# Performance work log

Hardware: AMD Instinct MI355X
Metric: run time of the kernel (lower is better)

## Reference

```python
import jax, jax.numpy as jnp
import numpy as np

DIM = 96
HEADS = 6
WS = 8                      # window_size
OWS = int(WS * 0.5) + WS    # overlap_win_size = 12
PAD = (OWS - WS) // 2       # 2
Dd = Hh = Ww = 24
B = 1
L = Dd * Hh * Ww
MLP_H = DIM * 2
TBL = (WS + OWS - 1) ** 3   # 6859 relative-position-bias entries


def setup_inputs() -> dict:
    key = jax.random.key(0)
    ks = jax.random.split(key, 8)
    def n(k, shape, s=0.02):
        return jax.random.normal(k, shape, jnp.float32) * s
    return {
        "x": jax.random.normal(ks[0], (B, L, DIM), jnp.float32),
        "ln1_w": jnp.ones((DIM,), jnp.float32),
        "ln1_b": jnp.zeros((DIM,), jnp.float32),
        "qkv_w": n(ks[1], (3 * DIM, DIM)),
        "qkv_b": jnp.zeros((3 * DIM,), jnp.float32),
        "rpb": n(ks[2], (TBL, HEADS)),
        "proj_w": n(ks[3], (DIM, DIM)),
        "proj_b": jnp.zeros((DIM,), jnp.float32),
        "ln2_w": jnp.ones((DIM,), jnp.float32),
        "ln2_b": jnp.zeros((DIM,), jnp.float32),
        "fc1_w": n(ks[4], (MLP_H, DIM)),
        "fc1_b": jnp.zeros((MLP_H,), jnp.float32),
        "fc2_w": n(ks[5], (DIM, MLP_H)),
        "fc2_b": jnp.zeros((DIM,), jnp.float32),
        "rpi": jax.random.randint(ks[6], (WS ** 3, OWS ** 3), 0, TBL),
        "D": Dd, "H": Hh, "W": Ww,
    }


def _ln(x, w, b):
    m = jnp.mean(x, -1, keepdims=True)
    v = jnp.var(x, -1, keepdims=True)
    return (x - m) / jnp.sqrt(v + 1e-5) * w + b


def _ocab3d(x, ln1_w, ln1_b, qkv_w, qkv_b, rpb, proj_w, proj_b,
            ln2_w, ln2_b, fc1_w, fc1_b, fc2_w, fc2_b, rpi, D, H, W):
    Bz, Lz, C = x.shape
    hd = C // HEADS
    scale = hd ** -0.5
    shortcut = x

    xn = _ln(x, ln1_w, ln1_b).reshape(Bz, D, H, W, C)
    qkv = xn @ qkv_w.T + qkv_b                   # [B,D,H,W,3C]
    q = qkv[..., :C]
    kv = qkv[..., C:]                            # cat(k, v) on channels, [B,D,H,W,2C]

    nD, nH, nW = D // WS, H // WS, W // WS
    nw = nD * nH * nW

    # non-overlapping query windows -> [B*nw, WS^3, C]
    qw = q.reshape(Bz, nD, WS, nH, WS, nW, WS, C)
    qw = qw.transpose(0, 1, 3, 5, 2, 4, 6, 7).reshape(Bz * nw, WS ** 3, C)

    # overlapping kv windows via pad + strided gather (mirrors F.pad + unfold)
    kvp = jnp.pad(kv, ((0, 0), (PAD, PAD), (PAD, PAD), (PAD, PAD), (0, 0)))
    idx_d = (jnp.arange(nD) * WS)[:, None] + jnp.arange(OWS)[None, :]
    idx_h = (jnp.arange(nH) * WS)[:, None] + jnp.arange(OWS)[None, :]
    idx_w = (jnp.arange(nW) * WS)[:, None] + jnp.arange(OWS)[None, :]
    kw = kvp[:, idx_d]                 # [B,nD,OWS,Hp,Wp,2C]
    kw = kw[:, :, :, idx_h]            # [B,nD,OWS,nH,OWS,Wp,2C]
    kw = kw[:, :, :, :, :, idx_w]      # [B,nD,OWS,nH,OWS,nW,OWS,2C]
    kw = kw.transpose(0, 1, 3, 5, 2, 4, 6, 7).reshape(Bz * nw, OWS ** 3, 2 * C)
    kk, vv = kw[..., :C], kw[..., C:]

    qh = qw.reshape(-1, WS ** 3, HEADS, hd).transpose(0, 2, 1, 3) * scale
    kh = kk.reshape(-1, OWS ** 3, HEADS, hd).transpose(0, 2, 1, 3)
    vh = vv.reshape(-1, OWS ** 3, HEADS, hd).transpose(0, 2, 1, 3)

    attn = jnp.einsum('bhqd,bhkd->bhqk', qh, kh)               # [B*nw,H,512,1728]
    bias = rpb[rpi.reshape(-1)].reshape(WS ** 3, OWS ** 3, HEADS).transpose(2, 0, 1)
    attn = jax.nn.softmax(attn + bias[None], axis=-1)
    out = jnp.einsum('bhqk,bhkd->bhqd', attn, vh)
    out = out.transpose(0, 2, 1, 3).reshape(Bz * nw, WS ** 3, C)

    # window reverse -> [B, L, C]
    out = out.reshape(Bz, nD, nH, nW, WS, WS, WS, C)
    out = out.transpose(0, 1, 4, 2, 5, 3, 6, 7).reshape(Bz, D * H * W, C)

    x2 = out @ proj_w.T + proj_b + shortcut
    h1 = jax.nn.gelu(_ln(x2, ln2_w, ln2_b) @ fc1_w.T + fc1_b, approximate=False)
    return x2 + (h1 @ fc2_w.T + fc2_b)


def reference(x, ln1_w, ln1_b, qkv_w, qkv_b, rpb, proj_w, proj_b,
              ln2_w, ln2_b, fc1_w, fc1_b, fc2_w, fc2_b, rpi, D, H, W):
    return _ocab3d(x, ln1_w, ln1_b, qkv_w, qkv_b, rpb, proj_w, proj_b,
                   ln2_w, ln2_b, fc1_w, fc1_b, fc2_w, fc2_b, rpi, D, H, W)
```

## Files before the change

kernel.cpp:

```cpp
#include <hip/hip_runtime.h>
#include <math.h>

#define DIMC   96
#define NHEADS 6
#define HD     16
#define WSZ    8
#define OWSZ   12
#define PADW   2
#define DD     24
#define LTOK   13824
#define NWIN   27
#define NKEY   1728
#define NROW   512
#define MLPH   192
#define PDIM   28
#define PD3    21952
#define TBL    6859
#define LSTR   82944
#define AOSTR  1327104
#define LOG2E  1.4426950408889634f

typedef __attribute__((ext_vector_type(4))) short bf16x4;
typedef __attribute__((ext_vector_type(8))) short bf16x8;
typedef __attribute__((ext_vector_type(4))) float f32x4;

__device__ __forceinline__ unsigned short bfround(float f) {
    unsigned u = __float_as_uint(f);
    return (unsigned short)((u + 0x7FFFu + ((u >> 16) & 1u)) >> 16);
}
__device__ __forceinline__ unsigned bfpack(float a, float b) {
    unsigned ua = __float_as_uint(a), ub = __float_as_uint(b);
    ua = (ua + 0x7FFFu + ((ua >> 16) & 1u)) >> 16;
    ub = (ub + 0x7FFFu + ((ub >> 16) & 1u)) >> 16;
    return ua | (ub << 16);
}
__device__ __forceinline__ uint4 pack8(const float* v) {
    uint4 u;
    u.x = bfpack(v[0], v[1]); u.y = bfpack(v[2], v[3]);
    u.z = bfpack(v[4], v[5]); u.w = bfpack(v[6], v[7]);
    return u;
}
__device__ __forceinline__ bf16x4 pack4(f32x4 p) {
    union { uint2 u; bf16x4 v; } r;
    r.u.x = __builtin_amdgcn_perm(__float_as_uint(p[1]), __float_as_uint(p[0]), 0x07060302u);
    r.u.y = __builtin_amdgcn_perm(__float_as_uint(p[3]), __float_as_uint(p[2]), 0x07060302u);
    return r.v;
}
__device__ __forceinline__ f32x4 cvt4(uint2 b) {
    f32x4 c;
    c[0] = __uint_as_float(b.x << 16);
    c[1] = __uint_as_float(b.x & 0xffff0000u);
    c[2] = __uint_as_float(b.y << 16);
    c[3] = __uint_as_float(b.y & 0xffff0000u);
    return c;
}
__device__ __forceinline__ f32x4 mfma16(bf16x4 a, bf16x4 b, f32x4 c) {
#if __has_builtin(__builtin_amdgcn_mfma_f32_16x16x16bf16_1k)
    return __builtin_amdgcn_mfma_f32_16x16x16bf16_1k(a, b, c, 0, 0, 0);
#else
    bf16x8 a8 = {a[0], a[1], a[2], a[3], 0, 0, 0, 0};
    bf16x8 b8 = {b[0], b[1], b[2], b[3], 0, 0, 0, 0};
    return __builtin_amdgcn_mfma_f32_16x16x32_bf16(a8, b8, c, 0, 0, 0);
#endif
}
__device__ __forceinline__ f32x4 mfma32k(bf16x8 a, bf16x8 b, f32x4 c) {
    return __builtin_amdgcn_mfma_f32_16x16x32_bf16(a, b, c, 0, 0, 0);
}
__device__ __forceinline__ float fexp2(float x) {
#if __has_builtin(__builtin_amdgcn_exp2f)
    return __builtin_amdgcn_exp2f(x);
#else
    return exp2f(x);
#endif
}

#define QKVB 1296
#define ZB   515
#define WPB  45
#define BIASB 216
__global__ __launch_bounds__(256) void qkvz_kernel(
        const float* __restrict__ X, const float* __restrict__ W,
        const float* __restrict__ bias, const float* __restrict__ lnw,
        const float* __restrict__ lnb,
        const float* __restrict__ projw, const float* __restrict__ fc1w,
        const float* __restrict__ fc2w,
        const int* __restrict__ rpi, const float* __restrict__ rpb,
        unsigned short* __restrict__ q16, unsigned short* __restrict__ kvp2,
        uint4* __restrict__ wpack, unsigned short* __restrict__ biasP) {
    __shared__ uint4 Af4[2 * 3 * 4 * 16];
    __shared__ uint4 Bf4[6 * 3 * 4 * 16];
    int bx = blockIdx.x, tid = threadIdx.x;

    if (bx >= QKVB + ZB + WPB) {
        int b2 = bx - (QKVB + ZB + WPB);
        int c  = b2 % 27;
        int qp = b2 / 27;
        int quart = qp >> 1, qt = qp & 1;
        int wavep = tid >> 6, quadp = (tid >> 4) & 3, m16p = tid & 15;
        int q = quart * 128 + wavep * 32 + qt * 16 + m16p;
        const int* rp = rpi + (long)q * NKEY + c * 64 + quadp * 8;
        #pragma unroll
        for (int kt = 0; kt < 4; ++kt) {
            int4 t = *(const int4*)(rp + (kt >> 1) * 32 + (kt & 1) * 4);
            const float2* p0 = (const float2*)(rpb + (long)t.x * 6);
            const float2* p1 = (const float2*)(rpb + (long)t.y * 6);
            const float2* p2 = (const float2*)(rpb + (long)t.z * 6);
            const float2* p3 = (const float2*)(rpb + (long)t.w * 6);
            #pragma unroll
            for (int hp = 0; hp < 3; ++hp) {
                float2 a0 = p0[hp], a1 = p1[hp], a2 = p2[hp], a3 = p3[hp];
                uint2 ua, ub;
                ua.x = bfpack(a0.x * LOG2E, a1.x * LOG2E);
                ua.y = bfpack(a2.x * LOG2E, a3.x * LOG2E);
                ub.x = bfpack(a0.y * LOG2E, a1.y * LOG2E);
                ub.y = bfpack(a2.y * LOG2E, a3.y * LOG2E);
                *(uint2*)(biasP + ((long)((2*hp)   * 4 + quart) * 27 + c) * 8192
                          + qt * 4096 + tid * 16 + kt * 4) = ua;
                *(uint2*)(biasP + ((long)((2*hp+1) * 4 + quart) * 27 + c) * 8192
                          + qt * 4096 + tid * 16 + kt * 4) = ub;
            }
        }
        return;
    }
    if (bx >= QKVB + ZB) {
        int u = (bx - QKVB - ZB) * 256 + tid;
        if (u < 5760) {
            int p = (u < 1152) ? u : (u < 3456 ? (u - 1152) % 1152 : (u - 3456) % 1152);
            int nn = p & 15, r = p >> 4, qg = r & 3, r2 = r >> 2;
            int kt = r2 % 3, ct = r2 / 3;
            int n = ct * 16 + nn, g = kt * 4 + qg;
            const float* src;
            if (u < 1152)      src = projw + n * 96 + g * 8;
            else if (u < 3456) { int nc = (u - 1152) / 1152; src = fc1w + (long)(nc * 96 + n) * 96 + g * 8; }
            else               { int kh = (u - 3456) / 1152; src = fc2w + (long)n * 192 + kh * 96 + g * 8; }
            const float4* s4 = (const float4*)src;
            float v[8];
            float4 t0 = s4[0], t1 = s4[1];
            v[0]=t0.x; v[1]=t0.y; v[2]=t0.z; v[3]=t0.w;
            v[4]=t1.x; v[5]=t1.y; v[6]=t1.z; v[7]=t1.w;
            wpack[u] = pack8(v);
        }
        return;
    }
    if (bx >= QKVB) {
        int t = (bx - QKVB) * 256 + tid;
        if (t < 21952 * 6) {
            int head = t / PD3, pos = t % PD3;
            int d = pos / 784, h = (pos / 28) % 28, w = pos % 28;
            if (d < 2 || d >= 26 || h < 2 || h >= 26 || w < 2 || w >= 26) {
                uint4* p = (uint4*)(kvp2 + ((long)head * PD3 + pos) * 32);
                uint4 z = make_uint4(0, 0, 0, 0);
                p[0] = z; p[1] = z; p[2] = z; p[3] = z;
            }
        }
        return;
    }

    int nc   = bx % 3;
    int row0 = (bx / 3) * 32;

    if (tid < 128) {
        int row = tid >> 2, part = tid & 3;
        int rt = row >> 4, mm = row & 15;
        float v[24];
        const float4* xp = (const float4*)(X + (long)(row0 + row) * 96 + part * 24);
        float s = 0.f, sq = 0.f;
        #pragma unroll
        for (int i = 0; i < 6; ++i) {
            float4 t = xp[i];
            v[i*4+0] = t.x; v[i*4+1] = t.y; v[i*4+2] = t.z; v[i*4+3] = t.w;
            s  += t.x + t.y + t.z + t.w;
            sq += t.x*t.x + t.y*t.y + t.z*t.z + t.w*t.w;
        }
        s  += __shfl_xor(s, 1);  s  += __shfl_xor(s, 2);
        sq += __shfl_xor(sq, 1); sq += __shfl_xor(sq, 2);
        float mean = s * (1.f / 96.f);
        float inv  = rsqrtf(sq * (1.f / 96.f) - mean * mean + 1e-5f);
        const float4* wp = (const float4*)(lnw + part * 24);
        const float4* bp = (const float4*)(lnb + part * 24);
        #pragma unroll
        for (int i = 0; i < 6; ++i) {
            float4 wv = wp[i], bv = bp[i];
            v[i*4+0] = (v[i*4+0] - mean) * inv * wv.x + bv.x;
            v[i*4+1] = (v[i*4+1] - mean) * inv * wv.y + bv.y;
            v[i*4+2] = (v[i*4+2] - mean) * inv * wv.z + bv.z;
            v[i*4+3] = (v[i*4+3] - mean) * inv * wv.w + bv.w;
        }
        #pragma unroll
        for (int gg = 0; gg < 3; ++gg) {
            int g = part * 3 + gg;
            int kt = g >> 2, qq = g & 3;
            Af4[((rt * 3 + kt) * 4 + qq) * 16 + mm] = pack8(v + gg * 8);
        }
    }
    for (int idx = tid; idx < 96 * 12; idx += 256) {
        int n = idx / 12;
        int g = idx % 12;
        const float4* wp = (const float4*)(W + (long)(nc * 96 + n) * 96 + g * 8);
        float v[8];
        float4 t0 = wp[0], t1 = wp[1];
        v[0]=t0.x; v[1]=t0.y; v[2]=t0.z; v[3]=t0.w;
        v[4]=t1.x; v[5]=t1.y; v[6]=t1.z; v[7]=t1.w;
        int ct = n >> 4, nn = n & 15, kt = g >> 2, qg = g & 3;
        Bf4[((ct * 3 + kt) * 4 + qg) * 16 + nn] = pack8(v);
    }
    __syncthreads();

    int wave = tid >> 6, lane = tid & 63;
    int qq = lane >> 4, mI = lane & 15;
    int rt = wave & 1, cg = wave >> 1;

    f32x4 acc[3];
    #pragma unroll
    for (int j = 0; j < 3; ++j) acc[j] = (f32x4){0.f, 0.f, 0.f, 0.f};
    #pragma unroll
    for (int kt = 0; kt < 3; ++kt) {
        bf16x8 a = *(const bf16x8*)&Af4[((rt * 3 + kt) * 4 + qq) * 16 + mI];
        #pragma unroll
        for (int j = 0; j < 3; ++j) {
            bf16x8 b = *(const bf16x8*)&Bf4[(((cg * 3 + j) * 3 + kt) * 4 + qq) * 16 + mI];
            acc[j] = __builtin_amdgcn_mfma_f32_16x16x32_bf16(a, b, acc[j], 0, 0, 0);
        }
    }

    float bv[3];
    #pragma unroll
    for (int j = 0; j < 3; ++j) bv[j] = bias[nc * 96 + (cg * 3 + j) * 16 + mI];
    #pragma unroll
    for (int r = 0; r < 4; ++r) {
        int row = row0 + rt * 16 + qq * 4 + r;
        if (nc == 0) {
            unsigned short* op = q16 + (long)row * 96;
            #pragma unroll
            for (int j = 0; j < 3; ++j)
                op[(cg * 3 + j) * 16 + mI] = bfround(0.25f * LOG2E * (acc[j][r] + bv[j]));
        } else {
            int d = row / 576, hh = (row / 24) % 24, w2 = row % 24;
            long pos = ((long)(d + 2) * 28 + (hh + 2)) * 28 + (w2 + 2);
            #pragma unroll
            for (int j = 0; j < 3; ++j) {
                int head = cg * 3 + j;
                kvp2[((long)head * PD3 + pos) * 32 +
                     (nc == 2 ? 16 : 0) + mI] = bfround(acc[j][r] + bv[j]);
            }
        }
    }
}

#define KSTR 20
#define VKP  66

#define ATTN_STEP(P, BCUR, BNXT)                                              \
    {                                                                         \
        bool more = (cc + (P) + 1 < cn);                                      \
        if (more) stgn = *kvaddr(c0 + cc + (P) + 1);                          \
        __syncthreads();                                                      \
        bf16x4 kf[4];                                                         \
        _Pragma("unroll")                                                     \
        for (int kt = 0; kt < 4; ++kt)                                        \
            kf[kt] = *(const bf16x4*)&Ks[(P)][(kt * 16 + m16) * KSTR + quad * 4]; \
        bf16x8 vb0 = *(const bf16x8*)&Vt[(P)][m16 * VKP + quad * 8];          \
        bf16x8 vb1 = *(const bf16x8*)&Vt[(P)][m16 * VKP + 32 + quad * 8];     \
        f32x4 S[2][4];                                                        \
        _Pragma("unroll")                                                     \
        for (int qt = 0; qt < 2; ++qt) {                                      \
            _Pragma("unroll")                                                 \
            for (int kt = 0; kt < 4; ++kt) {                                  \
                uint4 bj = BCUR[qt][kt >> 1];                                 \
                uint2 bb = (kt & 1) ? make_uint2(bj.z, bj.w)                  \
                                    : make_uint2(bj.x, bj.y);                 \
                S[qt][kt] = mfma16(kf[kt], qf[qt], cvt4(bb));                 \
            }                                                                 \
        }                                                                     \
        if (more) {                                                           \
            const unsigned short* bp = bbase + (long)(c0 + cc + (P) + 1) * 8192 \
                                       + tid * 16;                            \
            _Pragma("unroll")                                                 \
            for (int qt = 0; qt < 2; ++qt) {                                  \
                BNXT[qt][0] = *(const uint4*)(bp + qt * 4096);                \
                BNXT[qt][1] = *(const uint4*)(bp + qt * 4096 + 8);            \
            }                                                                 \
        }                                                                     \
        bf16x8 P8[2][2];                                                      \
        _Pragma("unroll")                                                     \
        for (int qt = 0; qt < 2; ++qt) {                                      \
            _Pragma("unroll")                                                 \
            for (int u = 0; u < 2; ++u) {                                     \
                f32x4 p0, p1;                                                 \
                _Pragma("unroll")                                             \
                for (int r = 0; r < 4; ++r) {                                 \
                    p0[r] = fexp2(S[qt][2 * u][r]);                           \
                    p1[r] = fexp2(S[qt][2 * u + 1][r]);                       \
                }                                                             \
                union { struct { bf16x4 lo, hi; } h; bf16x8 v; } uu;          \
                uu.h.lo = pack4(p0); uu.h.hi = pack4(p1);                     \
                P8[qt][u] = uu.v;                                             \
                lacc[qt] = mfma32k(P8[qt][u], ones8, lacc[qt]);               \
            }                                                                 \
        }                                                                     \
        o[0] = mfma32k(P8[0][0], vb0, o[0]);                                  \
        o[1] = mfma32k(P8[1][0], vb0, o[1]);                                  \
        o[0] = mfma32k(P8[0][1], vb1, o[0]);                                  \
        o[1] = mfma32k(P8[1][1], vb1, o[1]);                                  \
        if (more) writeLDS((P) ^ 1, stgn);                                    \
    }

__global__ __launch_bounds__(256, 3) void attn_kernel(
        const unsigned short* __restrict__ q, const unsigned short* __restrict__ kvp2,
        const unsigned short* __restrict__ biasP, float* __restrict__ ao,
        float* __restrict__ lbuf) {
    __shared__ unsigned short Ks[2][64 * KSTR];
    __shared__ unsigned short Vt[2][16 * VKP];
    int bid = blockIdx.x;
    int w = bid / 48, rem = bid % 48;
    int head = rem >> 3;
    int quart = (rem >> 1) & 3, half = rem & 1;
    int wd8 = (w / 9) * 8, wh8 = ((w / 3) % 3) * 8, ww8 = (w % 3) * 8;
    int tid = threadIdx.x, wave = tid >> 6, lane = tid & 63;
    int quad = lane >> 4, m16 = lane & 15;
    int key = tid >> 2, part = tid & 3;
    int c0 = half ? 13 : 0;
    int cn = half ? 14 : 13;

    int skey = (key & 35) | ((key & 4) << 2) | ((key >> 1) & 12);

    auto kvaddr = [&](int c) -> const uint4* {
        int jg = c * 64 + key;
        int i = jg / 144, jh = (jg / 12) % 12, jw = jg % 12;
        long sp = ((long)(wd8 + i) * PDIM + (wh8 + jh)) * PDIM + (ww8 + jw);
        return (const uint4*)(kvp2 + ((long)head * PD3 + sp) * 32 + part * 8);
    };
    auto writeLDS = [&](int b, uint4 v) {
        if (part < 2) {
            *(uint2*)(&Ks[b][skey * KSTR + part * 8])     = make_uint2(v.x, v.y);
            *(uint2*)(&Ks[b][skey * KSTR + part * 8 + 4]) = make_uint2(v.z, v.w);
        } else {
            int d0 = (part - 2) * 8;
            unsigned short* vp = &Vt[b][d0 * VKP + key];
            vp[0 * VKP] = (unsigned short)(v.x);
            vp[1 * VKP] = (unsigned short)(v.x >> 16);
            vp[2 * VKP] = (unsigned short)(v.y);
            vp[3 * VKP] = (unsigned short)(v.y >> 16);
            vp[4 * VKP] = (unsigned short)(v.z);
            vp[5 * VKP] = (unsigned short)(v.z >> 16);
            vp[6 * VKP] = (unsigned short)(v.w);
            vp[7 * VKP] = (unsigned short)(v.w >> 16);
        }
    };

    bf16x4 qf[2];
    #pragma unroll
    for (int qt = 0; qt < 2; ++qt) {
        int ql = quart * 128 + wave * 32 + qt * 16 + m16;
        int ld = ql >> 6, lh = (ql >> 3) & 7, lw = ql & 7;
        int g = ((wd8 + ld) * 24 + (wh8 + lh)) * 24 + (ww8 + lw);
        qf[qt] = *(const bf16x4*)(q + (long)g * 96 + head * 16 + quad * 4);
    }

    const unsigned short* bbase = biasP + ((long)(head * 4 + quart) * 27) * 8192;
    uint4 bb0[2][2], bb1[2][2];
    {
        const unsigned short* bp = bbase + (long)c0 * 8192 + tid * 16;
        #pragma unroll
        for (int qt = 0; qt < 2; ++qt) {
            bb0[qt][0] = *(const uint4*)(bp + qt * 4096);
            bb0[qt][1] = *(const uint4*)(bp + qt * 4096 + 8);
        }
    }

    writeLDS(0, *kvaddr(c0));

    const bf16x8 ones8 = {(short)0x3F80, (short)0x3F80, (short)0x3F80, (short)0x3F80,
                          (short)0x3F80, (short)0x3F80, (short)0x3F80, (short)0x3F80};
    f32x4 o[2], lacc[2];
    o[0] = (f32x4){0.f,0.f,0.f,0.f}; o[1] = (f32x4){0.f,0.f,0.f,0.f};
    lacc[0] = o[0]; lacc[1] = o[1];
    uint4 stgn;

    for (int cc = 0; cc < cn; cc += 2) {
        ATTN_STEP(0, bb0, bb1)
        if (cc + 1 < cn) ATTN_STEP(1, bb1, bb0)
    }

    float* aout = ao + (long)half * AOSTR;
    float* lout = lbuf + (long)half * LSTR;
    #pragma unroll
    for (int qt = 0; qt < 2; ++qt) {
        #pragma unroll
        for (int r = 0; r < 4; ++r) {
            int ql = quart * 128 + wave * 32 + qt * 16 + quad * 4 + r;
            int ld = ql >> 6, lh = (ql >> 3) & 7, lw = ql & 7;
            int g = ((wd8 + ld) * 24 + (wh8 + lh)) * 24 + (ww8 + lw);
            aout[(long)g * 96 + head * 16 + m16] = o[qt][r];
            if (m16 == 0) lout[g * 6 + head] = lacc[qt][r];
        }
    }
}

#define X2S 100
__global__ __launch_bounds__(512) void mlp_kernel(
        const float* __restrict__ ao0, const float* __restrict__ ao1,
        const float* __restrict__ lbuf, const uint4* __restrict__ wpack,
        const float* __restrict__ projb, const float* __restrict__ x,
        const float* __restrict__ ln2w, const float* __restrict__ ln2b,
        const float* __restrict__ fc1b, const float* __restrict__ fc2b,
        float* __restrict__ out) {
    __shared__ uint4 Ws[5760];
    __shared__ uint4 Af4[4 * 3 * 4 * 16];
    __shared__ float x2s[64 * X2S];
    __shared__ unsigned short h16[64 * 192];
    int tid = threadIdx.x;
    int row0 = blockIdx.x * 64;
    int wave = tid >> 6, lane = tid & 63;
    int qq = lane >> 4, mI = lane & 15;
    int rt = wave & 3, cg = wave >> 2;

    for (int idx = tid; idx < 5760; idx += 512) Ws[idx] = wpack[idx];

    if (tid < 256) {
        int row = tid >> 2, part = tid & 3;
        int rtA = row >> 4, mm = row & 15;
        int grow = row0 + row;
        const float4* a0 = (const float4*)(ao0 + (long)grow * 96 + part * 24);
        const float4* a1 = (const float4*)(ao1 + (long)grow * 96 + part * 24);
        int ha = (part * 3) >> 1, hb = ha + 1;
        float inva = 1.f / (lbuf[grow*6 + ha] + lbuf[LSTR + grow*6 + ha]);
        float invb = 1.f / (lbuf[grow*6 + hb] + lbuf[LSTR + grow*6 + hb]);
        float v[24];
        #pragma unroll
        for (int i = 0; i < 6; ++i) {
            float4 u0 = a0[i], u1 = a1[i];
            #pragma unroll
            for (int j = 0; j < 4; ++j) {
                int gc = part * 24 + i * 4 + j;
                float lv = ((gc >> 4) == ha) ? inva : invb;
                float s = (j==0?u0.x+u1.x : j==1?u0.y+u1.y : j==2?u0.z+u1.z : u0.w+u1.w);
                v[i*4+j] = s * lv;
            }
        }
        #pragma unroll
        for (int gg = 0; gg < 3; ++gg) {
            int g = part * 3 + gg;
            int kt = g >> 2, q4 = g & 3;
            Af4[((rtA * 3 + kt) * 4 + q4) * 16 + mm] = pack8(v + gg * 8);
        }
    }
    __syncthreads();

    {
        f32x4 acc[3];
        #pragma unroll
        for (int j = 0; j < 3; ++j) acc[j] = (f32x4){0.f,0.f,0.f,0.f};
        #pragma unroll
        for (int kt = 0; kt < 3; ++kt) {
            bf16x8 a = *(const bf16x8*)&Af4[((rt * 3 + kt) * 4 + qq) * 16 + mI];
            #pragma unroll
            for (int j = 0; j < 3; ++j) {
                bf16x8 b = *(const bf16x8*)&Ws[(((cg * 3 + j) * 3 + kt) * 4 + qq) * 16 + mI];
                acc[j] = __builtin_amdgcn_mfma_f32_16x16x32_bf16(a, b, acc[j], 0, 0, 0);
            }
        }
        float bv[3];
        #pragma unroll
        for (int j = 0; j < 3; ++j) bv[j] = projb[(cg * 3 + j) * 16 + mI];
        #pragma unroll
        for (int r = 0; r < 4; ++r) {
            int row = rt * 16 + qq * 4 + r;
            int grow = row0 + row;
            #pragma unroll
            for (int j = 0; j < 3; ++j) {
                int col = (cg * 3 + j) * 16 + mI;
                x2s[row * X2S + col] = acc[j][r] + bv[j] + x[(long)grow * 96 + col];
            }
        }
    }
    __syncthreads();

    if (tid < 256) {
        int row = tid >> 2, part = tid & 3;
        int rtA = row >> 4, mm = row & 15;
        float v[24];
        const float4* xp = (const float4*)(x2s + row * X2S + part * 24);
        float s = 0.f, sq = 0.f;
        #pragma unroll
        for (int i = 0; i < 6; ++i) {
            float4 t = xp[i];
            v[i*4+0] = t.x; v[i*4+1] = t.y; v[i*4+2] = t.z; v[i*4+3] = t.w;
            s  += t.x + t.y + t.z + t.w;
            sq += t.x*t.x + t.y*t.y + t.z*t.z + t.w*t.w;
        }
        s  += __shfl_xor(s, 1);  s  += __shfl_xor(s, 2);
        sq += __shfl_xor(sq, 1); sq += __shfl_xor(sq, 2);
        float mean = s * (1.f / 96.f);
        float inv  = rsqrtf(sq * (1.f / 96.f) - mean * mean + 1e-5f);
        const float4* wp = (const float4*)(ln2w + part * 24);
        const float4* bp = (const float4*)(ln2b + part * 24);
        #pragma unroll
        for (int i = 0; i < 6; ++i) {
            float4 wv = wp[i], bv = bp[i];
            v[i*4+0] = (v[i*4+0] - mean) * inv * wv.x + bv.x;
            v[i*4+1] = (v[i*4+1] - mean) * inv * wv.y + bv.y;
            v[i*4+2] = (v[i*4+2] - mean) * inv * wv.z + bv.z;
            v[i*4+3] = (v[i*4+3] - mean) * inv * wv.w + bv.w;
        }
        #pragma unroll
        for (int gg = 0; gg < 3; ++gg) {
            int g = part * 3 + gg;
            int kt = g >> 2, q4 = g & 3;
            Af4[((rtA * 3 + kt) * 4 + q4) * 16 + mm] = pack8(v + gg * 8);
        }
    }
    __syncthreads();

    #pragma unroll
    for (int nc = 0; nc < 2; ++nc) {
        f32x4 acc[3];
        #pragma unroll
        for (int j = 0; j < 3; ++j) acc[j] = (f32x4){0.f,0.f,0.f,0.f};
        #pragma unroll
        for (int kt = 0; kt < 3; ++kt) {
            bf16x8 a = *(const bf16x8*)&Af4[((rt * 3 + kt) * 4 + qq) * 16 + mI];
            #pragma unroll
            for (int j = 0; j < 3; ++j) {
                bf16x8 b = *(const bf16x8*)&Ws[1152 + nc * 1152 +
                               (((cg * 3 + j) * 3 + kt) * 4 + qq) * 16 + mI];
                acc[j] = __builtin_amdgcn_mfma_f32_16x16x32_bf16(a, b, acc[j], 0, 0, 0);
            }
        }
        float bv[3];
        #pragma unroll
        for (int j = 0; j < 3; ++j) bv[j] = fc1b[nc * 96 + (cg * 3 + j) * 16 + mI];
        #pragma unroll
        for (int r = 0; r < 4; ++r) {
            int row = rt * 16 + qq * 4 + r;
            #pragma unroll
            for (int j = 0; j < 3; ++j) {
                int col = nc * 96 + (cg * 3 + j) * 16 + mI;
                float v = acc[j][r] + bv[j];
                float g = 0.5f * v * (1.f + erff(v * 0.70710678f));
                int fi = (((row >> 4) * 6 + (col >> 5)) * 4 + ((col >> 3) & 3)) * 16 + (row & 15);
                h16[fi * 8 + (col & 7)] = bfround(g);
            }
        }
    }
    __syncthreads();

    f32x4 acc2[3];
    #pragma unroll
    for (int j = 0; j < 3; ++j) acc2[j] = (f32x4){0.f,0.f,0.f,0.f};
    #pragma unroll
    for (int kh = 0; kh < 2; ++kh) {
        #pragma unroll
        for (int kt = 0; kt < 3; ++kt) {
            int ktA = kh * 3 + kt;
            bf16x8 a = *(const bf16x8*)&h16[(((rt * 6 + ktA) * 4 + qq) * 16 + mI) * 8];
            #pragma unroll
            for (int j = 0; j < 3; ++j) {
                bf16x8 b = *(const bf16x8*)&Ws[3456 + kh * 1152 +
                               (((cg * 3 + j) * 3 + kt) * 4 + qq) * 16 + mI];
                acc2[j] = __builtin_amdgcn_mfma_f32_16x16x32_bf16(a, b, acc2[j], 0, 0, 0);
            }
        }
    }
    float bv[3];
    #pragma unroll
    for (int j = 0; j < 3; ++j) bv[j] = fc2b[(cg * 3 + j) * 16 + mI];
    #pragma unroll
    for (int r = 0; r < 4; ++r) {
        int row = rt * 16 + qq * 4 + r;
        int grow = row0 + row;
        #pragma unroll
        for (int j = 0; j < 3; ++j) {
            int col = (cg * 3 + j) * 16 + mI;
            out[(long)grow * 96 + col] = acc2[j][r] + bv[j] + x2s[row * X2S + col];
        }
    }
}

extern "C" void kernel_launch(void* const* d_in, const int* in_sizes, int n_in,
                              void* d_out, int out_size, void* d_ws, size_t ws_size,
                              hipStream_t stream) {
    const float* x     = (const float*)d_in[0];
    const float* ln1w  = (const float*)d_in[1];
    const float* ln1b  = (const float*)d_in[2];
    const float* qkvw  = (const float*)d_in[3];
    const float* qkvb  = (const float*)d_in[4];
    const float* rpb   = (const float*)d_in[5];
    const float* projw = (const float*)d_in[6];
    const float* projb = (const float*)d_in[7];
    const float* ln2w  = (const float*)d_in[8];
    const float* ln2b  = (const float*)d_in[9];
    const float* fc1w  = (const float*)d_in[10];
    const float* fc1b  = (const float*)d_in[11];
    const float* fc2w  = (const float*)d_in[12];
    const float* fc2b  = (const float*)d_in[13];
    const int*   rpi   = (const int*)d_in[14];
    float* outp = (float*)d_out;

    float* ws = (float*)d_ws;
    float*          aop    = ws;
    unsigned short* q16    = (unsigned short*)(ws + 2654208);
    unsigned short* kvp16  = (unsigned short*)(ws + 3317760);
    unsigned short* biasPh = (unsigned short*)(ws + 5425152);
    float*          lbuf   = ws + 10733568;
    uint4*          wpack  = (uint4*)(ws + 10899456);

    qkvz_kernel<<<QKVB + ZB + WPB + BIASB, 256, 0, stream>>>(
        x, qkvw, qkvb, ln1w, ln1b, projw, fc1w, fc2w, rpi, rpb,
        q16, kvp16, wpack, biasPh);
    attn_kernel<<<NWIN * NHEADS * 4 * 2, 256, 0, stream>>>(q16, kvp16, biasPh, aop, lbuf);
    mlp_kernel<<<LTOK / 64, 512, 0, stream>>>(aop, aop + AOSTR, lbuf, wpack, projb, x,
                                              ln2w, ln2b, fc1b, fc2b, outp);
}
```

Before: 158.8 us.

## Read MLP weights from global memory and shrink MLP blocks; vectorize bias gather

The MLP kernel no longer copies the full 92KB packed weight set into LDS per block. It reads B fragments directly from global memory (cached) and uses 32-row blocks of 256 threads, which lowers LDS use and should raise occupancy and block count. The bias-prep path now loads each 6-float rpb entry with one float4 plus one float2 and writes each head's 16 bf16 values as two uint4 stores instead of many uint2 stores. The tradeoff is repeated global/L2 reads of weights inside the MFMA loops, which may add latency.

Result: no change. 161.4 us (+1.6%).

```diff
diff --git a/kernel.cpp b/kernel.cpp
--- a/kernel.cpp
+++ b/kernel.cpp
@@ -96,29 +96,43 @@
         int c  = b2 % 27;
         int qp = b2 / 27;
         int quart = qp >> 1, qt = qp & 1;
-        int wavep = tid >> 6, quadp = (tid >> 4) & 3, m16p = tid & 15;
+        int quadp = (tid >> 4) & 3, m16p = tid & 15;
+        int wavep = tid >> 6;
         int q = quart * 128 + wavep * 32 + qt * 16 + m16p;
         const int* rp = rpi + (long)q * NKEY + c * 64 + quadp * 8;
+        uint2 h[6][4];
         #pragma unroll
         for (int kt = 0; kt < 4; ++kt) {
             int4 t = *(const int4*)(rp + (kt >> 1) * 32 + (kt & 1) * 4);
-            const float2* p0 = (const float2*)(rpb + (long)t.x * 6);
-            const float2* p1 = (const float2*)(rpb + (long)t.y * 6);
-            const float2* p2 = (const float2*)(rpb + (long)t.z * 6);
-            const float2* p3 = (const float2*)(rpb + (long)t.w * 6);
-            #pragma unroll
-            for (int hp = 0; hp < 3; ++hp) {
-                float2 a0 = p0[hp], a1 = p1[hp], a2 = p2[hp], a3 = p3[hp];
-                uint2 ua, ub;
-                ua.x = bfpack(a0.x * LOG2E, a1.x * LOG2E);
-                ua.y = bfpack(a2.x * LOG2E, a3.x * LOG2E);
-                ub.x = bfpack(a0.y * LOG2E, a1.y * LOG2E);
-                ub.y = bfpack(a2.y * LOG2E, a3.y * LOG2E);
-                *(uint2*)(biasP + ((long)((2*hp)   * 4 + quart) * 27 + c) * 8192
-                          + qt * 4096 + tid * 16 + kt * 4) = ua;
-                *(uint2*)(biasP + ((long)((2*hp+1) * 4 + quart) * 27 + c) * 8192
-                          + qt * 4096 + tid * 16 + kt * 4) = ub;
-            }
+            const float* b0 = rpb + (long)t.x * 6;
+            const float* b1 = rpb + (long)t.y * 6;
+            const float* b2p = rpb + (long)t.z * 6;
+            const float* b3 = rpb + (long)t.w * 6;
+            float4 q0 = *(const float4*)b0; float2 r0 = *(const float2*)(b0 + 4);
+            float4 q1 = *(const float4*)b1; float2 r1 = *(const float2*)(b1 + 4);
+            float4 q2 = *(const float4*)b2p; float2 r2 = *(const float2*)(b2p + 4);
+            float4 q3 = *(const float4*)b3; float2 r3 = *(const float2*)(b3 + 4);
+            h[0][kt].x = bfpack(q0.x * LOG2E, q1.x * LOG2E);
+            h[0][kt].y = bfpack(q2.x * LOG2E, q3.x * LOG2E);
+            h[1][kt].x = bfpack(q0.y * LOG2E, q1.y * LOG2E);
+            h[1][kt].y = bfpack(q2.y * LOG2E, q3.y * LOG2E);
+            h[2][kt].x = bfpack(q0.z * LOG2E, q1.z * LOG2E);
+            h[2][kt].y = bfpack(q2.z * LOG2E, q3.z * LOG2E);
+            h[3][kt].x = bfpack(q0.w * LOG2E, q1.w * LOG2E);
+            h[3][kt].y = bfpack(q2.w * LOG2E, q3.w * LOG2E);
+            h[4][kt].x = bfpack(r0.x * LOG2E, r1.x * LOG2E);
+            h[4][kt].y = bfpack(r2.x * LOG2E, r3.x * LOG2E);
+            h[5][kt].x = bfpack(r0.y * LOG2E, r1.y * LOG2E);
+            h[5][kt].y = bfpack(r2.y * LOG2E, r3.y * LOG2E);
+        }
+        long ob = qt * 4096 + tid * 16;
+        #pragma unroll
+        for (int head = 0; head < 6; ++head) {
+            unsigned short* o = biasP + ((long)(head * 4 + quart) * 27 + c) * 8192 + ob;
+            *(uint4*)(o)     = make_uint4(h[head][0].x, h[head][0].y,
+                                          h[head][1].x, h[head][1].y);
+            *(uint4*)(o + 8) = make_uint4(h[head][2].x, h[head][2].y,
+                                          h[head][3].x, h[head][3].y);
         }
         return;
     }
@@ -398,26 +412,23 @@
 }
 
 #define X2S 100
-__global__ __launch_bounds__(512) void mlp_kernel(
+__global__ __launch_bounds__(256) void mlp_kernel(
         const float* __restrict__ ao0, const float* __restrict__ ao1,
         const float* __restrict__ lbuf, const uint4* __restrict__ wpack,
         const float* __restrict__ projb, const float* __restrict__ x,
         const float* __restrict__ ln2w, const float* __restrict__ ln2b,
         const float* __restrict__ fc1b, const float* __restrict__ fc2b,
         float* __restrict__ out) {
-    __shared__ uint4 Ws[5760];
-    __shared__ uint4 Af4[4 * 3 * 4 * 16];
-    __shared__ float x2s[64 * X2S];
-    __shared__ unsigned short h16[64 * 192];
+    __shared__ uint4 Af4[2 * 3 * 4 * 16];
+    __shared__ float x2s[32 * X2S];
+    __shared__ unsigned short h16[32 * 192];
     int tid = threadIdx.x;
-    int row0 = blockIdx.x * 64;
+    int row0 = blockIdx.x * 32;
     int wave = tid >> 6, lane = tid & 63;
     int qq = lane >> 4, mI = lane & 15;
-    int rt = wave & 3, cg = wave >> 2;
-
-    for (int idx = tid; idx < 5760; idx += 512) Ws[idx] = wpack[idx];
-
-    if (tid < 256) {
+    int rt = wave & 1, cg = wave >> 1;
+
+    if (tid < 128) {
         int row = tid >> 2, part = tid & 3;
         int rtA = row >> 4, mm = row & 15;
         int grow = row0 + row;
@@ -456,7 +467,7 @@
             bf16x8 a = *(const bf16x8*)&Af4[((rt * 3 + kt) * 4 + qq) * 16 + mI];
             #pragma unroll
             for (int j = 0; j < 3; ++j) {
-                bf16x8 b = *(const bf16x8*)&Ws[(((cg * 3 + j) * 3 + kt) * 4 + qq) * 16 + mI];
+                bf16x8 b = *(const bf16x8*)&wpack[(((cg * 3 + j) * 3 + kt) * 4 + qq) * 16 + mI];
                 acc[j] = __builtin_amdgcn_mfma_f32_16x16x32_bf16(a, b, acc[j], 0, 0, 0);
             }
         }
@@ -476,7 +487,7 @@
     }
     __syncthreads();
 
-    if (tid < 256) {
+    if (tid < 128) {
         int row = tid >> 2, part = tid & 3;
         int rtA = row >> 4, mm = row & 15;
         float v[24];
@@ -522,7 +533,7 @@
             bf16x8 a = *(const bf16x8*)&Af4[((rt * 3 + kt) * 4 + qq) * 16 + mI];
             #pragma unroll
             for (int j = 0; j < 3; ++j) {
-                bf16x8 b = *(const bf16x8*)&Ws[1152 + nc * 1152 +
+                bf16x8 b = *(const bf16x8*)&wpack[1152 + nc * 1152 +
                                (((cg * 3 + j) * 3 + kt) * 4 + qq) * 16 + mI];
                 acc[j] = __builtin_amdgcn_mfma_f32_16x16x32_bf16(a, b, acc[j], 0, 0, 0);
             }
@@ -556,7 +567,7 @@
             bf16x8 a = *(const bf16x8*)&h16[(((rt * 6 + ktA) * 4 + qq) * 16 + mI) * 8];
             #pragma unroll
             for (int j = 0; j < 3; ++j) {
-                bf16x8 b = *(const bf16x8*)&Ws[3456 + kh * 1152 +
+                bf16x8 b = *(const bf16x8*)&wpack[3456 + kh * 1152 +
                                (((cg * 3 + j) * 3 + kt) * 4 + qq) * 16 + mI];
                 acc2[j] = __builtin_amdgcn_mfma_f32_16x16x32_bf16(a, b, acc2[j], 0, 0, 0);
             }
@@ -609,6 +620,6 @@
         x, qkvw, qkvb, ln1w, ln1b, projw, fc1w, fc2w, rpi, rpb,
         q16, kvp16, wpack, biasPh);
     attn_kernel<<<NWIN * NHEADS * 4 * 2, 256, 0, stream>>>(q16, kvp16, biasPh, aop, lbuf);
-    mlp_kernel<<<LTOK / 64, 512, 0, stream>>>(aop, aop + AOSTR, lbuf, wpack, projb, x,
+    mlp_kernel<<<LTOK / 32, 256, 0, stream>>>(aop, aop + AOSTR, lbuf, wpack, projb, x,
                                               ln2w, ln2b, fc1b, fc2b, outp);
 }
```
